# Performance work log

Hardware: AMD Instinct MI355X
Metric: run time of the kernel (lower is better)

## Reference

```python
import jax, jax.numpy as jnp
import numpy as np

EPS = 1e-5
BN_SCALE = 1.0 / np.sqrt(1.0 + EPS)  # inference BN with running_mean=0, running_var=1


def lrelu(x):
    return jnp.where(x >= 0, x, 0.2 * x)


def bn_affine(x, g, b, axis=1):
    shp = [1] * x.ndim
    shp[axis] = -1
    return x * (g.reshape(shp) * BN_SCALE) + b.reshape(shp)


def knn_idx(x, k):
    # x: (B, C, N) -> (B, N, k) indices of k nearest neighbors (incl. self)
    x2 = jnp.sum(x * x, axis=1)                       # (B, N)
    inner = jnp.einsum('bcn,bcm->bnm', x, x)          # (B, N, N)
    neg_dist = 2.0 * inner - x2[:, :, None] - x2[:, None, :]
    return jax.lax.top_k(neg_dist, k)[1]


def graph_feature(x, k):
    # x: (B, C, N) -> (B, 2C, N, k) edge features [x_j - x_i, x_i]
    B, C, N = x.shape
    idx = knn_idx(x, k)                               # (B, N, k)
    xt = jnp.transpose(x, (0, 2, 1))                  # (B, N, C)
    nbr = xt[jnp.arange(B)[:, None, None], idx]       # (B, N, k, C)
    ctr = xt[:, :, None, :]                           # (B, N, 1, C)
    feat = jnp.concatenate([nbr - ctr, jnp.broadcast_to(ctr, nbr.shape)], axis=-1)
    return jnp.transpose(feat, (0, 3, 1, 2))          # (B, 2C, N, k)


def edge_conv(x, W, g, b, k):
    # get_graph_feature -> 1x1 conv -> BN -> LeakyReLU -> max over neighbors
    f = graph_feature(x, k)
    h = jnp.einsum('oc,bcnk->bonk', W, f)
    return jnp.max(lrelu(bn_affine(h, g, b, axis=1)), axis=-1)  # (B, O, N)


def fps(xyz, m):
    # xyz: (B, 3, N) -> (B, m) farthest-point-sample indices, starting at index 0
    B, _, N = xyz.shape
    pts = jnp.transpose(xyz, (0, 2, 1))               # (B, N, 3)

    def body(carry, _):
        dists, last = carry
        p = jnp.take_along_axis(pts, last[:, None, None], axis=1)  # (B, 1, 3)
        d = jnp.sum((pts - p) ** 2, axis=-1)          # (B, N)
        dists = jnp.minimum(dists, d)
        nxt = jnp.argmax(dists, axis=-1).astype(jnp.int32)
        return (dists, nxt), last

    init = (jnp.full((B, N), 1e10, dtype=xyz.dtype), jnp.zeros((B,), jnp.int32))
    _, idxs = jax.lax.scan(body, init, None, length=m)
    return jnp.transpose(idxs, (1, 0))                # (B, m)


def gather_ch(x, idx):
    # x: (B, C, N), idx: (B, M) -> (B, C, M)
    B, C, _ = x.shape
    return jnp.take_along_axis(x, jnp.broadcast_to(idx[:, None, :], (B, C, idx.shape[1])), axis=2)


def aggregate(xyz, node, features, k):
    # xyz: (B,3,N), node: (B,3,M), features: (B,C,N) -> (B,C,M)
    B = xyz.shape[0]
    x2 = jnp.sum(xyz * xyz, axis=1)                   # (B, N)
    n2 = jnp.sum(node * node, axis=1)                 # (B, M)
    inner = jnp.einsum('bcm,bcn->bmn', node, xyz)     # (B, M, N)
    neg_d = 2.0 * inner - n2[:, :, None] - x2[:, None, :]
    idx = jax.lax.top_k(neg_d, k)[1]                  # (B, M, k) nearest points per node
    ft = jnp.transpose(features, (0, 2, 1))           # (B, N, C)
    grp = ft[jnp.arange(B)[:, None, None], idx]       # (B, M, k, C)
    return jnp.transpose(jnp.max(grp, axis=2), (0, 2, 1))  # (B, C, M)


def setup_inputs() -> dict:
    key = jax.random.key(0)
    ks = jax.random.split(key, 32)
    B, N, K, E = 8, 2048, 20, 1024

    def w(k_, o, c):
        return jax.random.normal(k_, (o, c), jnp.float32) / np.sqrt(c)

    def gb(k_, c):
        k1, k2 = jax.random.split(k_)
        return (jax.random.uniform(k1, (c,), jnp.float32, 0.5, 1.5),
                0.1 * jax.random.normal(k2, (c,), jnp.float32))

    g1, b1 = gb(ks[1], 64); g2, b2 = gb(ks[2], 64); g2m, b2m = gb(ks[3], E)
    g3, b3 = gb(ks[4], 256); g4, b4 = gb(ks[5], 256); g5, b5 = gb(ks[6], E)
    g6, b6 = gb(ks[7], 512); g7, b7 = gb(ks[8], 256)
    return {
        'x': jax.random.normal(ks[0], (B, 3, N), jnp.float32),
        'W1': w(ks[10], 64, 6), 'g1': g1, 'b1': b1,
        'W2': w(ks[11], 64, 128), 'g2': g2, 'b2': b2,
        'W2m': w(ks[12], E, 128), 'g2m': g2m, 'b2m': b2m,
        'W3': w(ks[13], 256, 512), 'g3': g3, 'b3': b3,
        'W4': w(ks[14], 256, 512), 'g4': g4, 'b4': b4,
        'W5': w(ks[15], E, 512), 'g5': g5, 'b5': b5,
        'Wl1': w(ks[16], 512, 2 * E), 'g6': g6, 'b6': b6,
        'Wl2': w(ks[17], 256, 512), 'bl2': 0.01 * jax.random.normal(ks[18], (256,), jnp.float32),
        'g7': g7, 'b7': b7,
        'Wl3': w(ks[19], 40, 256), 'bl3': 0.01 * jax.random.normal(ks[20], (40,), jnp.float32),
    }


def reference(x, W1, g1, b1, W2, g2, b2, W2m, g2m, b2m, W3, g3, b3,
              W4, g4, b4, W5, g5, b5, Wl1, g6, b6, Wl2, bl2, g7, b7, Wl3, bl3):
    K = 20
    B, _, N = x.shape
    xyz = x

    x1 = edge_conv(x, W1, g1, b1, K)                  # (B, 64, N)
    x2 = edge_conv(x1, W2, g2, b2, K)                 # (B, 64, N)
    xt1_ = jnp.concatenate([x1, x2], axis=1)          # (B, 128, N)
    xt1 = lrelu(bn_affine(jnp.einsum('oc,bcn->bon', W2m, xt1_), g2m, b2m, axis=1))

    idx = fps(xyz, N // 4)                            # (B, N/4)
    node1 = gather_ch(xyz, idx)                       # (B, 3, N/4)
    nf1 = gather_ch(xt1_, idx)                        # (B, 128, N/4)
    agg = aggregate(xyz, node1, xt1_, K)              # (B, 128, N/4)
    xm = jnp.concatenate([nf1, agg], axis=1)          # (B, 256, N/4)

    x3 = edge_conv(xm, W3, g3, b3, K // 2)            # (B, 256, N/4)
    x4 = edge_conv(x3, W4, g4, b4, K // 2)            # (B, 256, N/4)
    xt2 = lrelu(bn_affine(jnp.einsum('oc,bcn->bon', W5, jnp.concatenate([x3, x4], axis=1)), g5, b5, axis=1))

    v = jnp.concatenate([jnp.max(xt1, axis=-1), jnp.max(xt2, axis=-1)], axis=1)  # (B, 2E)
    h = lrelu(bn_affine(v @ Wl1.T, g6, b6, axis=1))   # dropout = identity (eval)
    h = lrelu(bn_affine(h @ Wl2.T + bl2, g7, b7, axis=1))
    logits = h @ Wl3.T + bl3                          # (B, 40)
    return (logits, node1)
```

## Files before the change

kernel.cpp:

```cpp
#include <hip/hip_runtime.h>

#define BN_SCALE 0.9999950000374997f

template <int CTRL>
__device__ __forceinline__ float dpp_fmax_step(float v) {
  int xi = __builtin_bit_cast(int, v);
  int ti = __builtin_amdgcn_update_dpp(xi, xi, CTRL, 0xf, 0xf, false);
  return fmaxf(v, __builtin_bit_cast(float, ti));
}
template <int CTRL>
__device__ __forceinline__ int dpp_imin_step(int v) {
  int t = __builtin_amdgcn_update_dpp(v, v, CTRL, 0xf, 0xf, false);
  return (t < v) ? t : v;
}
template <int CTRL>
__device__ __forceinline__ float dpp_fadd_step(float v) {
  int ti = __builtin_amdgcn_update_dpp(0, __builtin_bit_cast(int, v), CTRL, 0xf, 0xf, true);
  return v + __builtin_bit_cast(float, ti);
}
__device__ __forceinline__ float wave_fmax(float v) {
  v = dpp_fmax_step<0x111>(v);
  v = dpp_fmax_step<0x112>(v);
  v = dpp_fmax_step<0x114>(v);
  v = dpp_fmax_step<0x118>(v);
  v = dpp_fmax_step<0x142>(v);
  v = dpp_fmax_step<0x143>(v);
  return __builtin_bit_cast(float, __builtin_amdgcn_readlane(__builtin_bit_cast(int, v), 63));
}
__device__ __forceinline__ int wave_imin(int v) {
  v = dpp_imin_step<0x111>(v);
  v = dpp_imin_step<0x112>(v);
  v = dpp_imin_step<0x114>(v);
  v = dpp_imin_step<0x118>(v);
  v = dpp_imin_step<0x142>(v);
  v = dpp_imin_step<0x143>(v);
  return __builtin_amdgcn_readlane(v, 63);
}
__device__ __forceinline__ float wave_fadd(float v) {
  v = dpp_fadd_step<0x111>(v);
  v = dpp_fadd_step<0x112>(v);
  v = dpp_fadd_step<0x114>(v);
  v = dpp_fadd_step<0x118>(v);
  v = dpp_fadd_step<0x142>(v);
  v = dpp_fadd_step<0x143>(v);
  return __builtin_bit_cast(float, __builtin_amdgcn_readlane(__builtin_bit_cast(int, v), 63));
}

template <int R, bool SQPRE>
__device__ __forceinline__ void knn4_body(const float* __restrict__ Q, int qStrideB,
                                          const float* __restrict__ Xc, int cStrideB,
                                          int C, int M, int N, int k, int* __restrict__ idxOut,
                                          const float* __restrict__ sqPre,
                                          int b, int q0, char* smem) {
  constexpr int NR = 4 * R;
  float (*negd)[R * 256] = (float (*)[R * 256])smem;
  int tid = threadIdx.x;
  const float* qb = Q + (long)b * qStrideB + q0;
  const float* cb = Xc + (long)b * cStrideB;
  if constexpr (R % 4 == 0) {
    constexpr int H = R / 4;
    float d0[R], d1[R], d2[R], d3[R], sq[R];
    #pragma unroll
    for (int i = 0; i < R; ++i) { d0[i] = d1[i] = d2[i] = d3[i] = sq[i] = 0.f; }
    for (int c = 0; c < C; ++c) {
      float4 q4 = *(const float4*)(qb + (long)c * M);
      const float4* pc4 = (const float4*)(cb + (long)c * N);
      #pragma unroll
      for (int h = 0; h < H; ++h) {
        float4 xv = pc4[tid + 256 * h];
        if (!SQPRE) {
          sq[4 * h + 0] = fmaf(xv.x, xv.x, sq[4 * h + 0]);
          sq[4 * h + 1] = fmaf(xv.y, xv.y, sq[4 * h + 1]);
          sq[4 * h + 2] = fmaf(xv.z, xv.z, sq[4 * h + 2]);
          sq[4 * h + 3] = fmaf(xv.w, xv.w, sq[4 * h + 3]);
        }
        d0[4 * h + 0] = fmaf(q4.x, xv.x, d0[4 * h + 0]);
        d0[4 * h + 1] = fmaf(q4.x, xv.y, d0[4 * h + 1]);
        d0[4 * h + 2] = fmaf(q4.x, xv.z, d0[4 * h + 2]);
        d0[4 * h + 3] = fmaf(q4.x, xv.w, d0[4 * h + 3]);
        d1[4 * h + 0] = fmaf(q4.y, xv.x, d1[4 * h + 0]);
        d1[4 * h + 1] = fmaf(q4.y, xv.y, d1[4 * h + 1]);
        d1[4 * h + 2] = fmaf(q4.y, xv.z, d1[4 * h + 2]);
        d1[4 * h + 3] = fmaf(q4.y, xv.w, d1[4 * h + 3]);
        d2[4 * h + 0] = fmaf(q4.z, xv.x, d2[4 * h + 0]);
        d2[4 * h + 1] = fmaf(q4.z, xv.y, d2[4 * h + 1]);
        d2[4 * h + 2] = fmaf(q4.z, xv.z, d2[4 * h + 2]);
        d2[4 * h + 3] = fmaf(q4.z, xv.w, d2[4 * h + 3]);
        d3[4 * h + 0] = fmaf(q4.w, xv.x, d3[4 * h + 0]);
        d3[4 * h + 1] = fmaf(q4.w, xv.y, d3[4 * h + 1]);
        d3[4 * h + 2] = fmaf(q4.w, xv.z, d3[4 * h + 2]);
        d3[4 * h + 3] = fmaf(q4.w, xv.w, d3[4 * h + 3]);
      }
    }
    #pragma unroll
    for (int h = 0; h < H; ++h) {
      float4 s4;
      if (SQPRE) {
        s4 = ((const float4*)(sqPre + (long)b * N))[tid + 256 * h];
      } else {
        s4 = make_float4(sq[4 * h], sq[4 * h + 1], sq[4 * h + 2], sq[4 * h + 3]);
      }
      ((float4*)negd[0])[tid + 256 * h] =
          make_float4(2.f * d0[4 * h] - s4.x, 2.f * d0[4 * h + 1] - s4.y,
                      2.f * d0[4 * h + 2] - s4.z, 2.f * d0[4 * h + 3] - s4.w);
      ((float4*)negd[1])[tid + 256 * h] =
          make_float4(2.f * d1[4 * h] - s4.x, 2.f * d1[4 * h + 1] - s4.y,
                      2.f * d1[4 * h + 2] - s4.z, 2.f * d1[4 * h + 3] - s4.w);
      ((float4*)negd[2])[tid + 256 * h] =
          make_float4(2.f * d2[4 * h] - s4.x, 2.f * d2[4 * h + 1] - s4.y,
                      2.f * d2[4 * h + 2] - s4.z, 2.f * d2[4 * h + 3] - s4.w);
      ((float4*)negd[3])[tid + 256 * h] =
          make_float4(2.f * d3[4 * h] - s4.x, 2.f * d3[4 * h + 1] - s4.y,
                      2.f * d3[4 * h + 2] - s4.z, 2.f * d3[4 * h + 3] - s4.w);
    }
  } else {
    float d0[R], d1[R], d2[R], d3[R], sq[R];
    #pragma unroll
    for (int i = 0; i < R; ++i) { d0[i] = d1[i] = d2[i] = d3[i] = sq[i] = 0.f; }
    for (int c = 0; c < C; ++c) {
      float4 q4 = *(const float4*)(qb + (long)c * M);
      const float* pc = cb + (long)c * N;
      #pragma unroll
      for (int i = 0; i < R; ++i) {
        float xv = pc[tid + 256 * i];
        sq[i] = fmaf(xv, xv, sq[i]);
        d0[i] = fmaf(q4.x, xv, d0[i]);
        d1[i] = fmaf(q4.y, xv, d1[i]);
        d2[i] = fmaf(q4.z, xv, d2[i]);
        d3[i] = fmaf(q4.w, xv, d3[i]);
      }
    }
    #pragma unroll
    for (int i = 0; i < R; ++i) {
      int m = tid + 256 * i;
      negd[0][m] = 2.f * d0[i] - sq[i];
      negd[1][m] = 2.f * d1[i] - sq[i];
      negd[2][m] = 2.f * d2[i] - sq[i];
      negd[3][m] = 2.f * d3[i] - sq[i];
    }
  }
  __syncthreads();
  int lane = tid & 63, w = tid >> 6;
  const float* row = negd[w];
  int* outp = idxOut + ((long)b * M + (q0 + w)) * k;
  float v[NR];
  #pragma unroll
  for (int i = 0; i < NR; ++i) v[i] = row[lane + 64 * i];
  constexpr int G = NR / 4;
  float bv[G]; int br[G];
  #pragma unroll
  for (int g = 0; g < G; ++g) {
    float v0 = v[4 * g]; int r0 = 4 * g;
    #pragma unroll
    for (int j = 1; j < 4; ++j) {
      bool c = v[4 * g + j] > v0;
      v0 = c ? v[4 * g + j] : v0;
      r0 = c ? (4 * g + j) : r0;
    }
    bv[g] = v0; br[g] = r0;
  }
  for (int kk = 0; kk < k; ++kk) {
    float mv[G]; int mi[G];
    #pragma unroll
    for (int g = 0; g < G; ++g) { mv[g] = bv[g]; mi[g] = br[g]; }
    #pragma unroll
    for (int s = G >> 1; s >= 1; s >>= 1) {
      #pragma unroll
      for (int i = 0; i < s; ++i) {
        bool c = mv[2 * i] >= mv[2 * i + 1];
        mv[i] = c ? mv[2 * i] : mv[2 * i + 1];
        mi[i] = c ? mi[2 * i] : mi[2 * i + 1];
      }
    }
    float best = mv[0]; int ib = mi[0];
    int bi = (best > -INFINITY) ? (lane + (ib << 6)) : N;
    float gmax = wave_fmax(best);
    int cand = (best == gmax) ? bi : 0x7FFFFFFF;
    int big = wave_imin(cand);
    if (lane == 0) outp[kk] = big;
    int ri = big >> 6;
    bool mine = (lane == (big & 63));
    #pragma unroll
    for (int i = 0; i < NR; ++i)
      if (i == ri) v[i] = mine ? -INFINITY : v[i];
    int gi = ri >> 2;
    #pragma unroll
    for (int g = 0; g < G; ++g) {
      if (g == gi) {
        float v0 = v[4 * g]; int r0 = 4 * g;
        #pragma unroll
        for (int j = 1; j < 4; ++j) {
          bool c = v[4 * g + j] > v0;
          v0 = c ? v[4 * g + j] : v0;
          r0 = c ? (4 * g + j) : r0;
        }
        bv[g] = v0; br[g] = r0;
      }
    }
  }
}

template <int R>
__global__ void knn4_kernel(const float* __restrict__ Q, int qStrideB,
                            const float* __restrict__ Xc, int cStrideB,
                            int C, int M, int N, int k, int* __restrict__ idxOut) {
  __shared__ __align__(16) char smem[R * 256 * 4 * 4];
  knn4_body<R, false>(Q, qStrideB, Xc, cStrideB, C, M, N, k, idxOut, nullptr,
                      blockIdx.y, blockIdx.x * 4, smem);
}

__device__ __forceinline__ void gemmPS_body(const float* __restrict__ X, int xStrideB, int C, int Np,
                                            const float* __restrict__ W, int ldw, int O,
                                            float* __restrict__ PtT, float* __restrict__ StT,
                                            int b, int n0, int o0, char* smem) {
  float (*Wp)[68] = (float (*)[68])smem;
  float (*Ws)[68] = (float (*)[68])(smem + 4352);
  float (*Xt)[68] = (float (*)[68])(smem + 8704);
  int tid = threadIdx.x;
  int to = tid % 16, tn = tid / 16;
  float accP[4][4] = {}, accS[4][4] = {};
  for (int c0 = 0; c0 < C; c0 += 16) {
    for (int e = tid; e < 16 * 64; e += 256) {
      int oo = e / 16, kk = e % 16;
      int c = c0 + kk, o = o0 + oo;
      bool ok = (c < C && o < O);
      Wp[kk][oo] = ok ? W[(long)o * ldw + c] : 0.f;
      Ws[kk][oo] = ok ? W[(long)o * ldw + C + c] : 0.f;
    }
    for (int e = tid; e < 16 * 64; e += 256) {
      int kk = e / 64, nn = e % 64;
      int c = c0 + kk, n = n0 + nn;
      Xt[kk][nn] = (c < C && n < Np) ? X[(long)b * xStrideB + (long)c * Np + n] : 0.f;
    }
    __syncthreads();
    for (int kk = 0; kk < 16; ++kk) {
      float4 xv = *(const float4*)&Xt[kk][tn * 4];
      float4 wp = *(const float4*)&Wp[kk][to * 4];
      float4 ws = *(const float4*)&Ws[kk][to * 4];
      float xs[4] = {xv.x, xv.y, xv.z, xv.w};
      float wps[4] = {wp.x, wp.y, wp.z, wp.w};
      float wss[4] = {ws.x, ws.y, ws.z, ws.w};
      #pragma unroll
      for (int i = 0; i < 4; ++i)
        #pragma unroll
        for (int j = 0; j < 4; ++j) {
          accP[i][j] = fmaf(xs[i], wps[j], accP[i][j]);
          accS[i][j] = fmaf(xs[i], wss[j], accS[i][j]);
        }
    }
    __syncthreads();
  }
  #pragma unroll
  for (int i = 0; i < 4; ++i) {
    int n = n0 + tn * 4 + i;
    if (n >= Np) continue;
    int o = o0 + to * 4;
    if (o + 3 < O) {
      long off = ((long)b * Np + n) * O + o;
      *(float4*)&PtT[off] = make_float4(accP[i][0], accP[i][1], accP[i][2], accP[i][3]);
      *(float4*)&StT[off] = make_float4(accS[i][0], accS[i][1], accS[i][2], accS[i][3]);
    } else {
      for (int j = 0; j < 4; ++j) {
        int oo = o + j;
        if (oo < O) {
          long off = ((long)b * Np + n) * O + oo;
          PtT[off] = accP[i][j];
          StT[off] = accS[i][j];
        }
      }
    }
  }
}

__device__ __forceinline__ void ecfinish_body64(const float* __restrict__ Pt, const float* __restrict__ St,
                                                const int* __restrict__ idx, int k, int O, int Np,
                                                const float* __restrict__ g, const float* __restrict__ bb,
                                                float* __restrict__ outp, long oStrideB,
                                                float* __restrict__ sqOut,
                                                int b, int blk) {
  int tid = threadIdx.x;
  int o = tid & 63;
  int n = blk * 4 + (tid >> 6);
  const float* PtB = Pt + (long)b * Np * O;
  const float* StB = St + (long)b * Np * O;
  const int* ip = idx + ((long)b * Np + n) * k;
  float mx = -INFINITY, mn = INFINITY;
  for (int kk = 0; kk < k; ++kk) {
    float v = PtB[(long)ip[kk] * O + o];
    mx = fmaxf(mx, v); mn = fminf(mn, v);
  }
  float ctrP = PtB[(long)n * O + o];
  float ctrS = StB[(long)n * O + o];
  float gs = g[o] * BN_SCALE;
  float m = (gs >= 0.f) ? mx : mn;
  float h = (ctrS - ctrP + m) * gs + bb[o];
  float out = h >= 0.f ? h : 0.2f * h;
  outp[(long)b * oStrideB + (long)o * Np + n] = out;
  if (sqOut) {
    int obits = __builtin_bit_cast(int, out);
    float acc = 0.f;
    #pragma unroll
    for (int c = 0; c < 64; ++c) {
      float hv = __builtin_bit_cast(float, __builtin_amdgcn_readlane(obits, c));
      acc = fmaf(hv, hv, acc);
    }
    if (o == 0) sqOut[(long)b * Np + n] = acc;
  }
}

__global__ void ecfinish_kernel(const float* __restrict__ Pt, const float* __restrict__ St,
                                const int* __restrict__ idx, int k, int O, int Np,
                                const float* __restrict__ g, const float* __restrict__ bb,
                                float* __restrict__ outp, long oStrideB) {
  int b = blockIdx.y;
  int n = blockIdx.x * blockDim.y + threadIdx.y;
  int o = threadIdx.x;
  const float* PtB = Pt + (long)b * Np * O;
  const float* StB = St + (long)b * Np * O;
  const int* ip = idx + ((long)b * Np + n) * k;
  float mx = -INFINITY, mn = INFINITY;
  for (int kk = 0; kk < k; ++kk) {
    float v = PtB[(long)ip[kk] * O + o];
    mx = fmaxf(mx, v); mn = fminf(mn, v);
  }
  float ctrP = PtB[(long)n * O + o];
  float ctrS = StB[(long)n * O + o];
  float gs = g[o] * BN_SCALE;
  float m = (gs >= 0.f) ? mx : mn;
  float h = (ctrS - ctrP + m) * gs + bb[o];
  outp[(long)b * oStrideB + (long)o * Np + n] = h >= 0.f ? h : 0.2f * h;
}

__device__ __forceinline__ void gemm_colmax_body(const float* __restrict__ X, int xStrideB, int C, int Np,
                                                 const float* __restrict__ W, int ldw, int O,
                                                 const float* __restrict__ g, const float* __restrict__ bb,
                                                 float* __restrict__ partial,
                                                 int b, int n0, int o0, int nt, int nNT, char* smem) {
  float (*Wt)[68] = (float (*)[68])smem;
  float (*Xt)[68] = (float (*)[68])(smem + 4352);
  int tid = threadIdx.x;
  int to = tid % 16, tn = tid / 16;
  float acc[4][4] = {};
  for (int c0 = 0; c0 < C; c0 += 16) {
    for (int e = tid; e < 16 * 64; e += 256) {
      int oo = e / 16, kk = e % 16;
      int c = c0 + kk, o = o0 + oo;
      Wt[kk][oo] = (c < C && o < O) ? W[(long)o * ldw + c] : 0.f;
    }
    for (int e = tid; e < 16 * 64; e += 256) {
      int kk = e / 64, nn = e % 64;
      int c = c0 + kk, n = n0 + nn;
      Xt[kk][nn] = (c < C && n < Np) ? X[(long)b * xStrideB + (long)c * Np + n] : 0.f;
    }
    __syncthreads();
    for (int kk = 0; kk < 16; ++kk) {
      float4 xv = *(const float4*)&Xt[kk][tn * 4];
      float4 wv = *(const float4*)&Wt[kk][to * 4];
      float xs[4] = {xv.x, xv.y, xv.z, xv.w};
      float wvs[4] = {wv.x, wv.y, wv.z, wv.w};
      #pragma unroll
      for (int i = 0; i < 4; ++i)
        #pragma unroll
        for (int j = 0; j < 4; ++j) acc[i][j] = fmaf(xs[i], wvs[j], acc[i][j]);
    }
    __syncthreads();
  }
  float vm[4];
  #pragma unroll
  for (int j = 0; j < 4; ++j) {
    int o = o0 + to * 4 + j;
    float gs = g[o] * BN_SCALE, bo = bb[o];
    float m = -INFINITY;
    #pragma unroll
    for (int i = 0; i < 4; ++i) {
      float h = acc[i][j] * gs + bo;
      h = h >= 0.f ? h : 0.2f * h;
      m = fmaxf(m, h);
    }
    vm[j] = m;
  }
  #pragma unroll
  for (int j = 0; j < 4; ++j) Xt[tn][to * 4 + j] = vm[j];
  __syncthreads();
  for (int s = 8; s > 0; s >>= 1) {
    if (tn < s)
      for (int j = 0; j < 4; ++j)
        Xt[tn][to * 4 + j] = fmaxf(Xt[tn][to * 4 + j], Xt[tn + s][to * 4 + j]);
    __syncthreads();
  }
  if (tn == 0)
    for (int j = 0; j < 4; ++j) {
      int o = o0 + to * 4 + j;
      partial[((long)b * nNT + nt) * O + o] = Xt[0][to * 4 + j];
    }
}

__global__ void gemm_colmax_kernel(const float* __restrict__ X, int xStrideB, int C, int Np,
                                   const float* __restrict__ W, int ldw, int O,
                                   const float* __restrict__ g, const float* __restrict__ bb,
                                   float* __restrict__ partial) {
  __shared__ __align__(16) char smem[8704];
  gemm_colmax_body(X, xStrideB, C, Np, W, ldw, O, g, bb, partial,
                   blockIdx.z, blockIdx.x * 64, blockIdx.y * 64, blockIdx.x, gridDim.x, smem);
}

__device__ __forceinline__ void xmfill_body(const float* __restrict__ xt1, int N,
                                            const int* __restrict__ fpsI,
                                            const int* __restrict__ idxA, int k, int M,
                                            float* __restrict__ xm, int xe) {
  long t = (long)xe * 256 + threadIdx.x;
  int i = (int)(t % M);
  int c = (int)((t / M) % 128);
  int b = (int)(t / ((long)128 * M));
  const float* xb = xt1 + (long)b * 128 * N + (long)c * N;
  float* xmB = xm + (long)b * 256 * M;
  xmB[(long)c * M + i] = xb[fpsI[(long)b * M + i]];
  const int* ip = idxA + ((long)b * M + i) * k;
  float best = -INFINITY;
  for (int kk = 0; kk < k; ++kk) best = fmaxf(best, xb[ip[kk]]);
  xmB[(long)(128 + c) * M + i] = best;
}

template <int FIRST, int LAST>
__device__ __forceinline__ void fps_body_rg(const float* __restrict__ xyz, int N, int M,
                                            int it0, int it1,
                                            int* __restrict__ fpsIdx, float* __restrict__ node1,
                                            float* __restrict__ distSv, int* __restrict__ lastSv,
                                            int b, char* smem) {
  #pragma clang fp contract(off)
  float* px = (float*)smem;
  float* py = (float*)(smem + 8192);
  float* pz = (float*)(smem + 16384);
  int*   fidx = (int*)(smem + 24576);
  float4* wvc = (float4*)(smem + 26624);
  int*   wis  = (int*)(smem + 26752);
  int tid = threadIdx.x;
  int lane = tid & 63, w = tid >> 6;
  const float* xb = xyz + (long)b * 3 * N;
  for (int n = tid; n < N; n += 256) {
    int s = ((n & 7) << 8) | (n >> 3);
    px[s] = xb[n]; py[s] = xb[N + n]; pz[s] = xb[2 * N + n];
  }
  if (!FIRST) {
    for (int e = tid; e < it0; e += 256) fidx[e] = fpsIdx[(long)b * M + e];
  }
  __syncthreads();
  float ptx[8], pty[8], ptz[8];
  #pragma unroll
  for (int i = 0; i < 8; ++i) {
    int s = (i << 8) | tid;
    ptx[i] = px[s]; pty[i] = py[s]; ptz[i] = pz[s];
  }
  float dist[8];
  int last;
  float lx, ly, lz;
  if (FIRST) {
    #pragma unroll
    for (int i = 0; i < 8; ++i) dist[i] = 1e10f;
    last = 0;
    int s0 = 0;
    lx = px[s0]; ly = py[s0]; lz = pz[s0];
  } else {
    #pragma unroll
    for (int i = 0; i < 8; ++i) dist[i] = distSv[(long)b * 2048 + i * 256 + tid];
    last = lastSv[b];
    int sl = ((last & 7) << 8) | (last >> 3);
    lx = px[sl]; ly = py[sl]; lz = pz[sl];
  }
  int base = tid * 8;
  for (int it = it0; it < it1; ++it) {
    int p = it & 1;
    if (tid == 0) fidx[it] = last;
    float best = -INFINITY; int bi = N;
    #pragma unroll
    for (int i = 0; i < 8; ++i) {
      float dx = ptx[i] - lx, dy = pty[i] - ly, dz = ptz[i] - lz;
      float dx2 = dx * dx, dy2 = dy * dy, dz2 = dz * dz;
      float d = (dx2 + dy2) + dz2;
      float dn = dist[i];
      if (d < dn) dn = d;
      dist[i] = dn;
      if (dn > best) { best = dn; bi = base + i; }
    }
    float cx = ptx[0], cy = pty[0], cz = ptz[0];
    #pragma unroll
    for (int i = 1; i < 8; ++i) {
      bool c = (bi == base + i);
      cx = c ? ptx[i] : cx; cy = c ? pty[i] : cy; cz = c ? ptz[i] : cz;
    }
    float gmax = wave_fmax(best);
    int cand = (best == gmax) ? bi : 0x7FFFFFFF;
    int wbi = wave_imin(cand);
    if (bi == wbi) { wvc[p * 4 + w] = make_float4(gmax, cx, cy, cz); wis[p * 4 + w] = wbi; }
    __syncthreads();
    float4 c0 = wvc[p * 4 + 0], c1 = wvc[p * 4 + 1], c2 = wvc[p * 4 + 2], c3 = wvc[p * 4 + 3];
    int i0 = wis[p * 4 + 0], i1 = wis[p * 4 + 1], i2 = wis[p * 4 + 2], i3 = wis[p * 4 + 3];
    float bv = c0.x; int bbi = i0; lx = c0.y; ly = c0.z; lz = c0.w;
    { bool c = (c1.x > bv) || (c1.x == bv && i1 < bbi);
      bv = c ? c1.x : bv; bbi = c ? i1 : bbi; lx = c ? c1.y : lx; ly = c ? c1.z : ly; lz = c ? c1.w : lz; }
    { bool c = (c2.x > bv) || (c2.x == bv && i2 < bbi);
      bv = c ? c2.x : bv; bbi = c ? i2 : bbi; lx = c ? c2.y : lx; ly = c ? c2.z : ly; lz = c ? c2.w : lz; }
    { bool c = (c3.x > bv) || (c3.x == bv && i3 < bbi);
      bv = c ? c3.x : bv; bbi = c ? i3 : bbi; lx = c ? c3.y : lx; ly = c ? c3.z : ly; lz = c ? c3.w : lz; }
    last = bbi;
  }
  if (!LAST) {
    for (int e = tid; e < it1; e += 256) {
      if (e >= it0) fpsIdx[(long)b * M + e] = fidx[e];
    }
    #pragma unroll
    for (int i = 0; i < 8; ++i) distSv[(long)b * 2048 + i * 256 + tid] = dist[i];
    if (tid == 0) lastSv[b] = last;
  } else {
    for (int e = tid; e < M; e += 256) fpsIdx[(long)b * M + e] = fidx[e];
    for (int e = tid; e < 3 * M; e += 256) {
      int c = e / M, i = e % M;
      int src = fidx[i];
      int s = ((src & 7) << 8) | (src >> 3);
      node1[(long)b * 3 * M + e] = (c == 0) ? px[s] : (c == 1) ? py[s] : pz[s];
    }
  }
}

template <int FIRST, int LAST, bool SQP>
__global__ void knnfpsgemm_kernel(const float* __restrict__ Q, int qStrideB,
                                  const float* __restrict__ Xc, int cStrideB,
                                  int C, int Mq, int N, int k, int* __restrict__ idxOut,
                                  const float* __restrict__ W, int ldw, int O,
                                  float* __restrict__ Pt, float* __restrict__ St,
                                  const float* __restrict__ xyz, int Mf, int it0, int it1,
                                  int* __restrict__ fpsIdx, float* __restrict__ node1,
                                  float* __restrict__ distSv, int* __restrict__ lastSv,
                                  const float* __restrict__ sqPre,
                                  int nQblk, int nGblk, int nB) {
  __shared__ __align__(16) char smem[32768];
  int bid = blockIdx.x;
  if (bid < nB) {
    __builtin_amdgcn_s_setprio(1);
    fps_body_rg<FIRST, LAST>(xyz, N, Mf, it0, it1, fpsIdx, node1, distSv, lastSv, bid, smem);
    __builtin_amdgcn_s_setprio(0);
  } else if (bid < nB + nB * nQblk) {
    int e = bid - nB;
    knn4_body<8, SQP>(Q, qStrideB, Xc, cStrideB, C, Mq, N, k, idxOut, sqPre,
                      e / nQblk, (e % nQblk) * 4, smem);
  } else {
    int e = bid - nB - nB * nQblk;
    gemmPS_body(Xc, cStrideB, C, N, W, ldw, O, Pt, St,
                e / nGblk, (e % nGblk) * 64, 0, smem);
  }
}

__global__ void ecfps_kernel(const float* __restrict__ Pt, const float* __restrict__ St,
                             const int* __restrict__ idx, int k, int O, int Np,
                             const float* __restrict__ g, const float* __restrict__ bb,
                             float* __restrict__ outp, long oStrideB,
                             float* __restrict__ sqOut,
                             const float* __restrict__ xyz, int N, int Mf, int it0, int it1,
                             int* __restrict__ fpsIdx, float* __restrict__ node1,
                             float* __restrict__ distSv, int* __restrict__ lastSv,
                             int nEperB, int nB) {
  __shared__ __align__(16) char smem[26784];
  int bid = blockIdx.x;
  if (bid < nB) {
    __builtin_amdgcn_s_setprio(1);
    fps_body_rg<0, 0>(xyz, N, Mf, it0, it1, fpsIdx, node1, distSv, lastSv, bid, smem);
    __builtin_amdgcn_s_setprio(0);
  } else {
    int e = bid - nB;
    ecfinish_body64(Pt, St, idx, k, O, Np, g, bb, outp, oStrideB, sqOut,
                    e / nEperB, e % nEperB);
  }
}

__global__ void ecfagg_kernel(const float* __restrict__ Pt, const float* __restrict__ St,
                              const int* __restrict__ idxS2, int k2, int O2, int Np2,
                              const float* __restrict__ g2, const float* __restrict__ b2,
                              float* __restrict__ out2, long oStrideB2,
                              const float* __restrict__ Qn, int qStrideB,
                              const float* __restrict__ Xc, int cStrideB,
                              int Cq, int Mq, int Nc, int kq, int* __restrict__ idxAgg,
                              int nQblk, int nEperB) {
  __shared__ __align__(16) char smem[32768];
  int bid = blockIdx.x;
  if (bid % 5 == 0) {
    int a = bid / 5;
    knn4_body<8, false>(Qn, qStrideB, Xc, cStrideB, Cq, Mq, Nc, kq, idxAgg, nullptr,
                        a / nQblk, (a % nQblk) * 4, smem);
  } else {
    int e = bid - bid / 5 - 1;
    ecfinish_body64(Pt, St, idxS2, k2, O2, Np2, g2, b2, out2, oStrideB2, nullptr,
                    e / nEperB, e % nEperB);
  }
}

__global__ void colmaxxm_kernel(const float* __restrict__ X, int xStrideB, int C, int Np,
                                const float* __restrict__ W, int ldw, int O,
                                const float* __restrict__ g, const float* __restrict__ bb,
                                float* __restrict__ partial, int nNT, int nOT,
                                const float* __restrict__ xt1, int N,
                                const int* __restrict__ fpsI, const int* __restrict__ idxA,
                                int kq, int M, float* __restrict__ xm) {
  __shared__ __align__(16) char smem[8704];
  int bid = blockIdx.x;
  if (bid % 3 == 0) {
    xmfill_body(xt1, N, fpsI, idxA, kq, M, xm, bid / 3);
  } else {
    int e = bid - bid / 3 - 1;
    int per = nNT * nOT;
    int b = e / per, r = e % per;
    int nt = r % nNT, ot = r / nNT;
    gemm_colmax_body(X, xStrideB, C, Np, W, ldw, O, g, bb, partial,
                     b, nt * 64, ot * 64, nt, nNT, smem);
  }
}

__global__ void knngemm_kernel(const float* __restrict__ Xin, int xStrideB,
                               int C, int Mq, int N, int k, int* __restrict__ idxOut,
                               const float* __restrict__ W, int ldw, int O,
                               float* __restrict__ Pt, float* __restrict__ St,
                               int nQblk, int nGn, int nGo, int nB) {
  __shared__ __align__(16) char smem[13056];
  int bid = blockIdx.x;
  if (bid < nB * nQblk) {
    knn4_body<2, false>(Xin, xStrideB, Xin, xStrideB, C, Mq, N, k, idxOut, nullptr,
                        bid / nQblk, (bid % nQblk) * 4, smem);
  } else {
    int e = bid - nB * nQblk;
    int per = nGn * nGo;
    int b = e / per, r = e % per;
    int nt = r % nGn, ot = r / nGn;
    gemmPS_body(Xin, xStrideB, C, N, W, ldw, O, Pt, St, b, nt * 64, ot * 64, smem);
  }
}

__global__ void head_kernel(const float* __restrict__ partA, int NTa,
                            const float* __restrict__ partB, int NTb,
                            const float* __restrict__ Wl1, const float* __restrict__ g6, const float* __restrict__ b6,
                            const float* __restrict__ Wl2, const float* __restrict__ bl2,
                            const float* __restrict__ g7, const float* __restrict__ b7,
                            const float* __restrict__ Wl3, const float* __restrict__ bl3,
                            float* __restrict__ logits) {
  __shared__ float v[2048];
  __shared__ float h1[512];
  __shared__ float h2[256];
  int b = blockIdx.x, tid = threadIdx.x;
  int lane = tid & 63, w = tid >> 6;
  for (int o = tid; o < 1024; o += 256) {
    float m = -INFINITY;
    for (int t = 0; t < NTa; ++t) m = fmaxf(m, partA[((long)b * NTa + t) * 1024 + o]);
    v[o] = m;
    float m2 = -INFINITY;
    for (int t = 0; t < NTb; ++t) m2 = fmaxf(m2, partB[((long)b * NTb + t) * 1024 + o]);
    v[1024 + o] = m2;
  }
  __syncthreads();
  for (int o = w; o < 512; o += 4) {
    const float4* wr = (const float4*)(Wl1 + (long)o * 2048);
    const float4* vp = (const float4*)v;
    float s = 0.f;
    #pragma unroll
    for (int j = 0; j < 8; ++j) {
      float4 w4 = wr[lane + 64 * j];
      float4 v4 = vp[lane + 64 * j];
      s = fmaf(w4.x, v4.x, s); s = fmaf(w4.y, v4.y, s);
      s = fmaf(w4.z, v4.z, s); s = fmaf(w4.w, v4.w, s);
    }
    float t = wave_fadd(s);
    if (lane == 0) {
      float h = t * (g6[o] * BN_SCALE) + b6[o];
      h1[o] = h >= 0.f ? h : 0.2f * h;
    }
  }
  __syncthreads();
  for (int o = w; o < 256; o += 4) {
    const float4* wr = (const float4*)(Wl2 + (long)o * 512);
    const float4* hp = (const float4*)h1;
    float s = 0.f;
    #pragma unroll
    for (int j = 0; j < 2; ++j) {
      float4 w4 = wr[lane + 64 * j];
      float4 v4 = hp[lane + 64 * j];
      s = fmaf(w4.x, v4.x, s); s = fmaf(w4.y, v4.y, s);
      s = fmaf(w4.z, v4.z, s); s = fmaf(w4.w, v4.w, s);
    }
    float t = wave_fadd(s);
    if (lane == 0) {
      float sb = t + bl2[o];
      float h = sb * (g7[o] * BN_SCALE) + b7[o];
      h2[o] = h >= 0.f ? h : 0.2f * h;
    }
  }
  __syncthreads();
  for (int o = w; o < 40; o += 4) {
    const float4* wr = (const float4*)(Wl3 + (long)o * 256);
    const float4* hp = (const float4*)h2;
    float4 w4 = wr[lane];
    float4 v4 = hp[lane];
    float s = fmaf(w4.x, v4.x, 0.f);
    s = fmaf(w4.y, v4.y, s); s = fmaf(w4.z, v4.z, s); s = fmaf(w4.w, v4.w, s);
    float t = wave_fadd(s);
    if (lane == 0) logits[(long)b * 40 + o] = t + bl3[o];
  }
}

extern "C" void kernel_launch(void* const* d_in, const int* in_sizes, int n_in,
                              void* d_out, int out_size, void* d_ws, size_t ws_size,
                              hipStream_t stream) {
  const float* x   = (const float*)d_in[0];
  const float* W1  = (const float*)d_in[1];
  const float* g1  = (const float*)d_in[2];
  const float* b1  = (const float*)d_in[3];
  const float* W2  = (const float*)d_in[4];
  const float* g2  = (const float*)d_in[5];
  const float* b2  = (const float*)d_in[6];
  const float* W2m = (const float*)d_in[7];
  const float* g2m = (const float*)d_in[8];
  const float* b2m = (const float*)d_in[9];
  const float* W3  = (const float*)d_in[10];
  const float* g3  = (const float*)d_in[11];
  const float* b3  = (const float*)d_in[12];
  const float* W4  = (const float*)d_in[13];
  const float* g4  = (const float*)d_in[14];
  const float* b4  = (const float*)d_in[15];
  const float* W5  = (const float*)d_in[16];
  const float* g5  = (const float*)d_in[17];
  const float* b5  = (const float*)d_in[18];
  const float* Wl1 = (const float*)d_in[19];
  const float* g6  = (const float*)d_in[20];
  const float* b6  = (const float*)d_in[21];
  const float* Wl2 = (const float*)d_in[22];
  const float* bl2 = (const float*)d_in[23];
  const float* g7  = (const float*)d_in[24];
  const float* b7  = (const float*)d_in[25];
  const float* Wl3 = (const float*)d_in[26];
  const float* bl3 = (const float*)d_in[27];
  float* outF = (float*)d_out;

  const int B = 8, N = 2048, K = 20, M = 512, K2 = 10;

  float* ws    = (float*)d_ws;
  float* xt1   = ws;
  float* xm    = xt1 + (size_t)B * 128 * N;
  float* xc    = xm  + (size_t)B * 256 * M;
  float* Pt    = xc  + (size_t)B * 512 * M;
  float* St    = Pt  + (size_t)B * N * 64;
  float* partA = St  + (size_t)B * N * 64;
  float* partB = partA + (size_t)B * 32 * 1024;
  int*   idxK  = (int*)(partB + (size_t)B * 8 * 1024);
  int*   fpsI  = idxK + (size_t)B * N * K;
  float* fpsDist = (float*)(fpsI + (size_t)B * M);
  int*   fpsLast = (int*)(fpsDist + (size_t)B * 2048);
  int*   idxAgg  = fpsLast + 64;
  float* sqS2    = (float*)(idxAgg + (size_t)B * M * K);

  float* logits = outF;
  float* node1  = outF + 320;

  dim3 t256(256);
  const int nQblk = N / 4;
  const int nGblk = N / 64;
  const int nFused = B + B * nQblk + B * nGblk;
  const int nQa = M / 4;
  const int IT1 = 208, IT2 = 304;

  knnfpsgemm_kernel<1, 0, false><<<dim3(nFused), t256, 0, stream>>>(
      x, 3 * N, x, 3 * N, 3, N, N, K, idxK,
      W1, 6, 64, Pt, St,
      x, M, 0, IT1, fpsI, node1, fpsDist, fpsLast, nullptr, nQblk, nGblk, B);

  ecfps_kernel<<<dim3(B + B * (N / 4)), t256, 0, stream>>>(
      Pt, St, idxK, K, 64, N, g1, b1, xt1, (long)128 * N, sqS2,
      x, N, M, IT1, IT2, fpsI, node1, fpsDist, fpsLast, N / 4, B);

  knnfpsgemm_kernel<0, 1, true><<<dim3(nFused), t256, 0, stream>>>(
      xt1, 128 * N, xt1, 128 * N, 64, N, N, K, idxK,
      W2, 128, 64, Pt, St,
      x, M, IT2, M, fpsI, node1, fpsDist, fpsLast, sqS2, nQblk, nGblk, B);

  ecfagg_kernel<<<dim3(B * nQa + B * (N / 4)), t256, 0, stream>>>(
      Pt, St, idxK, K, 64, N, g2, b2, xt1 + (size_t)64 * N, (long)128 * N,
      node1, 3 * M, x, 3 * N, 3, M, N, K, idxAgg, nQa, N / 4);

  colmaxxm_kernel<<<dim3((B * 128 * M) / 256 + B * 32 * 16), t256, 0, stream>>>(
      xt1, 128 * N, 128, N, W2m, 128, 1024, g2m, b2m, partA, 32, 16,
      xt1, N, fpsI, idxAgg, K, M, xm);

  knngemm_kernel<<<dim3(B * nQa + B * (M / 64) * (256 / 64)), t256, 0, stream>>>(
      xm, 256 * M, 256, M, M, K2, idxK, W3, 512, 256, Pt, St, nQa, M / 64, 256 / 64, B);
  ecfinish_kernel<<<dim3(M, B), dim3(256, 1), 0, stream>>>(Pt, St, idxK, K2, 256, M, g3, b3, xc, (long)512 * M);

  knngemm_kernel<<<dim3(B * nQa + B * (M / 64) * (256 / 64)), t256, 0, stream>>>(
      xc, 512 * M, 256, M, M, K2, idxK, W4, 512, 256, Pt, St, nQa, M / 64, 256 / 64, B);
  ecfinish_kernel<<<dim3(M, B), dim3(256, 1), 0, stream>>>(Pt, St, idxK, K2, 256, M, g4, b4,
                                                           xc + (size_t)256 * M, (long)512 * M);

  gemm_colmax_kernel<<<dim3(M / 64, 1024 / 64, B), t256, 0, stream>>>(xc, 512 * M, 512, M, W5, 512, 1024,
                                                                      g5, b5, partB);

  head_kernel<<<dim3(B), t256, 0, stream>>>(partA, N / 64, partB, M / 64,
                                            Wl1, g6, b6, Wl2, bl2, g7, b7, Wl3, bl3, logits);
}
```

Measured before the change: 1.057 ms.

## Split classifier head into per-layer kernels parallel over output neurons

The single 8-block head kernel is split into four kernels: a column-max reduction, then two FC layers spread over 64 and 32 blocks that each load a weight row once and reuse it across all 8 batch items, then the final logits layer. This aims to stop the 4MB Wl1 read from being serialized over only 8 blocks and being re-read per batch. It adds three extra kernel launches and round trips of intermediates through global memory.

```diff
diff --git a/kernel.cpp b/kernel.cpp
--- a/kernel.cpp
+++ b/kernel.cpp
@@ -633,69 +633,94 @@
   }
 }
 
-__global__ void head_kernel(const float* __restrict__ partA, int NTa,
-                            const float* __restrict__ partB, int NTb,
-                            const float* __restrict__ Wl1, const float* __restrict__ g6, const float* __restrict__ b6,
-                            const float* __restrict__ Wl2, const float* __restrict__ bl2,
-                            const float* __restrict__ g7, const float* __restrict__ b7,
-                            const float* __restrict__ Wl3, const float* __restrict__ bl3,
-                            float* __restrict__ logits) {
-  __shared__ float v[2048];
-  __shared__ float h1[512];
-  __shared__ float h2[256];
+__global__ void headv_kernel(const float* __restrict__ partA, int NTa,
+                             const float* __restrict__ partB, int NTb,
+                             float* __restrict__ vws) {
   int b = blockIdx.x, tid = threadIdx.x;
-  int lane = tid & 63, w = tid >> 6;
   for (int o = tid; o < 1024; o += 256) {
     float m = -INFINITY;
     for (int t = 0; t < NTa; ++t) m = fmaxf(m, partA[((long)b * NTa + t) * 1024 + o]);
-    v[o] = m;
+    vws[(long)b * 2048 + o] = m;
     float m2 = -INFINITY;
     for (int t = 0; t < NTb; ++t) m2 = fmaxf(m2, partB[((long)b * NTb + t) * 1024 + o]);
-    v[1024 + o] = m2;
-  }
-  __syncthreads();
-  for (int o = w; o < 512; o += 4) {
+    vws[(long)b * 2048 + 1024 + o] = m2;
+  }
+}
+
+__global__ void headl1_kernel(const float* __restrict__ vws,
+                              const float* __restrict__ Wl1, const float* __restrict__ g6,
+                              const float* __restrict__ b6, float* __restrict__ h1ws) {
+  int tid = threadIdx.x;
+  int lane = tid & 63, w = tid >> 6;
+  int o0 = blockIdx.x * 8;
+  for (int oo = w; oo < 8; oo += 4) {
+    int o = o0 + oo;
     const float4* wr = (const float4*)(Wl1 + (long)o * 2048);
-    const float4* vp = (const float4*)v;
-    float s = 0.f;
-    #pragma unroll
-    for (int j = 0; j < 8; ++j) {
-      float4 w4 = wr[lane + 64 * j];
-      float4 v4 = vp[lane + 64 * j];
-      s = fmaf(w4.x, v4.x, s); s = fmaf(w4.y, v4.y, s);
-      s = fmaf(w4.z, v4.z, s); s = fmaf(w4.w, v4.w, s);
-    }
-    float t = wave_fadd(s);
-    if (lane == 0) {
-      float h = t * (g6[o] * BN_SCALE) + b6[o];
-      h1[o] = h >= 0.f ? h : 0.2f * h;
-    }
-  }
-  __syncthreads();
-  for (int o = w; o < 256; o += 4) {
+    float4 w4[8];
+    #pragma unroll
+    for (int j = 0; j < 8; ++j) w4[j] = wr[lane + 64 * j];
+    float gs = g6[o] * BN_SCALE, bo = b6[o];
+    for (int b = 0; b < 8; ++b) {
+      const float4* vp = (const float4*)(vws + (long)b * 2048);
+      float s = 0.f;
+      #pragma unroll
+      for (int j = 0; j < 8; ++j) {
+        float4 v4 = vp[lane + 64 * j];
+        s = fmaf(w4[j].x, v4.x, s); s = fmaf(w4[j].y, v4.y, s);
+        s = fmaf(w4[j].z, v4.z, s); s = fmaf(w4[j].w, v4.w, s);
+      }
+      float t = wave_fadd(s);
+      if (lane == 0) {
+        float h = t * gs + bo;
+        h1ws[(long)b * 512 + o] = h >= 0.f ? h : 0.2f * h;
+      }
+    }
+  }
+}
+
+__global__ void headl2_kernel(const float* __restrict__ h1ws,
+                              const float* __restrict__ Wl2, const float* __restrict__ bl2,
+                              const float* __restrict__ g7, const float* __restrict__ b7,
+                              float* __restrict__ h2ws) {
+  int tid = threadIdx.x;
+  int lane = tid & 63, w = tid >> 6;
+  int o0 = blockIdx.x * 8;
+  for (int oo = w; oo < 8; oo += 4) {
+    int o = o0 + oo;
     const float4* wr = (const float4*)(Wl2 + (long)o * 512);
-    const float4* hp = (const float4*)h1;
-    float s = 0.f;
-    #pragma unroll
-    for (int j = 0; j < 2; ++j) {
-      float4 w4 = wr[lane + 64 * j];
-      float4 v4 = hp[lane + 64 * j];
-      s = fmaf(w4.x, v4.x, s); s = fmaf(w4.y, v4.y, s);
-      s = fmaf(w4.z, v4.z, s); s = fmaf(w4.w, v4.w, s);
-    }
-    float t = wave_fadd(s);
-    if (lane == 0) {
-      float sb = t + bl2[o];
-      float h = sb * (g7[o] * BN_SCALE) + b7[o];
-      h2[o] = h >= 0.f ? h : 0.2f * h;
-    }
-  }
-  __syncthreads();
+    float4 w4[2];
+    #pragma unroll
+    for (int j = 0; j < 2; ++j) w4[j] = wr[lane + 64 * j];
+    float bl = bl2[o], gs = g7[o] * BN_SCALE, bo = b7[o];
+    for (int b = 0; b < 8; ++b) {
+      const float4* hp = (const float4*)(h1ws + (long)b * 512);
+      float s = 0.f;
+      #pragma unroll
+      for (int j = 0; j < 2; ++j) {
+        float4 v4 = hp[lane + 64 * j];
+        s = fmaf(w4[j].x, v4.x, s); s = fmaf(w4[j].y, v4.y, s);
+        s = fmaf(w4[j].z, v4.z, s); s = fmaf(w4[j].w, v4.w, s);
+      }
+      float t = wave_fadd(s);
+      if (lane == 0) {
+        float sb = t + bl;
+        float h = sb * gs + bo;
+        h2ws[(long)b * 256 + o] = h >= 0.f ? h : 0.2f * h;
+      }
+    }
+  }
+}
+
+__global__ void headl3_kernel(const float* __restrict__ h2ws,
+                              const float* __restrict__ Wl3, const float* __restrict__ bl3,
+                              float* __restrict__ logits) {
+  int b = blockIdx.x, tid = threadIdx.x;
+  int lane = tid & 63, w = tid >> 6;
+  const float4* hp = (const float4*)(h2ws + (long)b * 256);
+  float4 v4 = hp[lane];
   for (int o = w; o < 40; o += 4) {
     const float4* wr = (const float4*)(Wl3 + (long)o * 256);
-    const float4* hp = (const float4*)h2;
     float4 w4 = wr[lane];
-    float4 v4 = hp[lane];
     float s = fmaf(w4.x, v4.x, 0.f);
     s = fmaf(w4.y, v4.y, s); s = fmaf(w4.z, v4.z, s); s = fmaf(w4.w, v4.w, s);
     float t = wave_fadd(s);
@@ -752,6 +777,9 @@
   int*   fpsLast = (int*)(fpsDist + (size_t)B * 2048);
   int*   idxAgg  = fpsLast + 64;
   float* sqS2    = (float*)(idxAgg + (size_t)B * M * K);
+  float* vws     = sqS2 + (size_t)B * N;
+  float* h1ws    = vws + (size_t)B * 2048;
+  float* h2ws    = h1ws + (size_t)B * 512;
 
   float* logits = outF;
   float* node1  = outF + 320;
@@ -797,6 +825,8 @@
   gemm_colmax_kernel<<<dim3(M / 64, 1024 / 64, B), t256, 0, stream>>>(xc, 512 * M, 512, M, W5, 512, 1024,
                                                                       g5, b5, partB);
 
-  head_kernel<<<dim3(B), t256, 0, stream>>>(partA, N / 64, partB, M / 64,
-                                            Wl1, g6, b6, Wl2, bl2, g7, b7, Wl3, bl3, logits);
-}
+  headv_kernel<<<dim3(B), t256, 0, stream>>>(partA, N / 64, partB, M / 64, vws);
+  headl1_kernel<<<dim3(64), t256, 0, stream>>>(vws, Wl1, g6, b6, h1ws);
+  headl2_kernel<<<dim3(32), t256, 0, stream>>>(h1ws, Wl2, bl2, g7, b7, h2ws);
+  headl3_kernel<<<dim3(B), t256, 0, stream>>>(h2ws, Wl3, bl3, logits);
+}
```

Measured after the change: 984.4 us. -6.9%, faster.
